# Optimization experiments

Measured on AMD Instinct MI355X. Metric: run time of the kernel, lower is better.

The kernel has to match this reference:

```python
import jax, jax.numpy as jnp
import numpy as np

F_DIM = 256; L = 4; B = 1; H = 160; W = 160; FH = 1024; N = B * H * W

def _ln(x, w, b):
    mu = jnp.mean(x, -1, keepdims=True)
    var = jnp.mean(jnp.square(x - mu), -1, keepdims=True)
    return (x - mu) * jax.lax.rsqrt(var + 1e-5) * w + b

def _conv(x, w, b, groups=1, pad=0):
    y = jax.lax.conv_general_dilated(x, w, (1, 1), [(pad, pad), (pad, pad)],
                                     dimension_numbers=('NCHW', 'OIHW', 'NCHW'),
                                     feature_group_count=groups)
    return y + b[None, :, None, None]

def _wsilu(x):
    return jax.nn.sigmoid(4.0 * x) * x

def setup_inputs() -> dict:
    key = jax.random.key(0)
    ks = iter(jax.random.split(key, 40))
    nk = lambda: next(ks)
    s = 1.0 / np.sqrt(F_DIM).astype(np.float32)
    inp = {}
    inp['x'] = jax.random.normal(nk(), (B, 1, H, W), jnp.float32)
    inp['cin_w1'] = jax.random.normal(nk(), (F_DIM, 1, 1, 1), jnp.float32)
    inp['cin_b1'] = jnp.zeros((F_DIM,), jnp.float32)
    inp['cin_w2'] = jax.random.normal(nk(), (F_DIM, 1, 7, 7), jnp.float32) * 0.15
    inp['cin_b2'] = jnp.zeros((F_DIM,), jnp.float32)
    inp['ln0_w'] = jnp.ones((F_DIM,), jnp.float32); inp['ln0_b'] = jnp.zeros((F_DIM,), jnp.float32)
    inp['ln1_w'] = jnp.ones((L, F_DIM), jnp.float32); inp['ln1_b'] = jnp.zeros((L, F_DIM), jnp.float32)
    inp['ln2_w'] = jnp.ones((L, F_DIM), jnp.float32); inp['ln2_b'] = jnp.zeros((L, F_DIM), jnp.float32)
    for n in ['att_tmk', 'att_tmv', 'att_tmr', 'ffn_tmk', 'ffn_tmr']:
        inp[n] = jax.random.uniform(nk(), (L, F_DIM), jnp.float32)
    inp['att_tf'] = jax.random.normal(nk(), (L, F_DIM), jnp.float32) * 0.5
    # time_decay is stored as -exp(raw) by the module's loader
    inp['att_td'] = -jnp.exp(jax.random.normal(nk(), (L, F_DIM), jnp.float32) * 0.5)
    for n in ['att_kw', 'att_vw', 'att_rw', 'att_ow', 'ffn_rw']:
        inp[n] = jax.random.normal(nk(), (L, F_DIM, F_DIM), jnp.float32) * s
    inp['ffn_kw'] = jax.random.normal(nk(), (L, FH, F_DIM), jnp.float32) * s
    inp['ffn_vw'] = jax.random.normal(nk(), (L, F_DIM, FH), jnp.float32) * (1.0 / np.sqrt(FH).astype(np.float32))
    inp['spa_dw_w'] = jax.random.normal(nk(), (L, F_DIM, 1, 7, 7), jnp.float32) * 0.15
    inp['spa_dw_b'] = jnp.zeros((L, F_DIM), jnp.float32)
    inp['spa_pw_w'] = jax.random.normal(nk(), (L, F_DIM, F_DIM, 1, 1), jnp.float32) * s
    inp['spa_pw_b'] = jnp.zeros((L, F_DIM), jnp.float32)
    st = jnp.zeros((5 * L, N, F_DIM), jnp.float32)
    st = st.at[4::5].add(-1e30)  # pp slots start at -1e30 as in torch init
    inp['state0'] = st
    return inp

def reference(x, cin_w1, cin_b1, cin_w2, cin_b2, ln0_w, ln0_b, ln1_w, ln1_b,
              ln2_w, ln2_b, att_tmk, att_tmv, att_tmr, att_tf, att_td,
              att_kw, att_vw, att_rw, att_ow, ffn_tmk, ffn_tmr, ffn_kw,
              ffn_vw, ffn_rw, spa_dw_w, spa_dw_b, spa_pw_w, spa_pw_b, state0):
    # conv stem: 1x1 -> depthwise 7x7 -> WSiLU
    d = _conv(x, cin_w1, cin_b1)
    d = _wsilu(_conv(d, cin_w2, cin_b2, groups=F_DIM, pad=3))
    d = d.transpose(0, 2, 3, 1).reshape(N, F_DIM)  # 'b f h w -> (b h w) f'
    for i in range(L):
        if i == 0:
            d = _ln(d, ln0_w, ln0_b)
        # --- SA: single-step RWKV WKV ---
        xs = _ln(d, ln1_w[i], ln1_b[i])
        sp = state0[5 * i + 1]
        aa = state0[5 * i + 2]; bb = state0[5 * i + 3]; pp = state0[5 * i + 4]
        xk = xs * att_tmk[i] + sp * (1 - att_tmk[i])
        xv = xs * att_tmv[i] + sp * (1 - att_tmv[i])
        xr = xs * att_tmr[i] + sp * (1 - att_tmr[i])
        r = jax.nn.sigmoid(xr @ att_rw[i].T)
        k = xk @ att_kw[i].T
        v = xv @ att_vw[i].T
        ww = att_tf[i] + k
        p = jnp.maximum(pp, ww)
        e1 = jnp.exp(pp - p); e2 = jnp.exp(ww - p)
        wkv = (e1 * aa + e2 * v) / (e1 * bb + e2)
        d = d + (r * wkv) @ att_ow[i].T
        # --- FF: squared-relu channel mix ---
        xs = _ln(d, ln2_w[i], ln2_b[i])
        sp = state0[5 * i + 0]
        xk = xs * ffn_tmk[i] + sp * (1 - ffn_tmk[i])
        xr = xs * ffn_tmr[i] + sp * (1 - ffn_tmr[i])
        rr = jax.nn.sigmoid(xr @ ffn_rw[i].T)
        kk = jnp.square(jax.nn.relu(xk @ ffn_kw[i].T))
        d = d + rr * (kk @ ffn_vw[i].T)
        # --- spatial residual block ---
        img = d.reshape(B, H, W, F_DIM).transpose(0, 3, 1, 2)
        img = img + _conv(_conv(img, spa_dw_w[i], spa_dw_b[i], groups=F_DIM, pad=3),
                          spa_pw_w[i], spa_pw_b[i])
        d = img.transpose(0, 2, 3, 1).reshape(N, F_DIM)
    return d.reshape(B, H, W, F_DIM).transpose(0, 3, 1, 2)
```

## Files before the change

### kernel.cpp

```cpp
#include <hip/hip_runtime.h>
#include <hip/hip_bf16.h>
#include <cstdint>
#include <cstddef>

#define F_DIMC 256
#define FHC    1024
#define IMGH   160
#define IMGW   160
#define NTOK   25600
#define NLAY   4

using bf16 = __hip_bfloat16;
using f16  = _Float16;
typedef __attribute__((ext_vector_type(8))) short bf16x8;
typedef __attribute__((ext_vector_type(4))) float f32x4;

#define MFMA16(a, b, c) __builtin_amdgcn_mfma_f32_16x16x32_bf16((a), (b), (c), 0, 0, 0)

union H4 { f16 h[4]; uint2 u; };
union Pack4 { bf16 h[4]; uint2 u; };

__global__ void cvt_sp_k(const float* __restrict__ state0, bf16* __restrict__ spb)
{
    const size_t NF = (size_t)NTOK * F_DIMC;
    int y = blockIdx.y;
    int slot = (y < 4) ? 5 * y + 1 : 5 * (y - 4);
    size_t e = ((size_t)blockIdx.x * 256 + threadIdx.x) * 4;
    f32x4 v = *(const f32x4*)(state0 + (size_t)slot * NF + e);
    Pack4 p;
    #pragma unroll
    for (int j = 0; j < 4; ++j) p.h[j] = __float2bfloat16(v[j]);
    *(uint2*)(spb + (size_t)y * NF + e) = p.u;
}

__global__ void prep_mix_k(const float* __restrict__ kw, const float* __restrict__ vw,
                           const float* __restrict__ rw, const float* __restrict__ tmk,
                           const float* __restrict__ tmv, const float* __restrict__ tmr,
                           const float* __restrict__ fkw, const float* __restrict__ ftmk,
                           const float* __restrict__ frw, const float* __restrict__ ftmr,
                           bf16* __restrict__ Wcat, bf16* __restrict__ fkw2,
                           bf16* __restrict__ frw2)
{
    int l = blockIdx.y;
    int idx = blockIdx.x * 256 + threadIdx.x;
    int c = idx & 511, cc = c & 255;
    bool hi2 = c >= 256;
    int r = idx >> 9;
    if (r < 768) {
        const float* W; const float* T; int rr = r;
        if (r < 256)      { W = kw; T = tmk; }
        else if (r < 512) { W = vw; T = tmv; rr = r - 256; }
        else              { W = rw; T = tmr; rr = r - 512; }
        float w = W[(size_t)l * 65536 + rr * 256 + cc];
        float t = T[l * 256 + cc];
        Wcat[(size_t)l * 768 * 512 + (size_t)r * 512 + c] = __float2bfloat16(w * (hi2 ? 1.f - t : t));
    } else if (r < 1792) {
        int rr = r - 768;
        float w = fkw[(size_t)l * 1024 * 256 + rr * 256 + cc];
        float t = ftmk[l * 256 + cc];
        fkw2[(size_t)l * 1024 * 512 + (size_t)rr * 512 + c] = __float2bfloat16(w * (hi2 ? 1.f - t : t));
    } else {
        int rr = r - 1792;
        float w = frw[(size_t)l * 65536 + rr * 256 + cc];
        float t = ftmr[l * 256 + cc];
        frw2[(size_t)l * 256 * 512 + (size_t)rr * 512 + c] = __float2bfloat16(w * (hi2 ? 1.f - t : t));
    }
}

__global__ void cvt3_k(const float* __restrict__ ow, const float* __restrict__ pw,
                       const float* __restrict__ fvw, const float* __restrict__ dww,
                       bf16* __restrict__ owb, bf16* __restrict__ pwb,
                       bf16* __restrict__ fvwb, float* __restrict__ dwT)
{
    int z = blockIdx.y;
    int i = blockIdx.x * 256 + threadIdx.x;
    if (z == 0)      { if (i < 262144)  owb[i]  = __float2bfloat16(ow[i]); }
    else if (z == 1) { if (i < 262144)  pwb[i]  = __float2bfloat16(pw[i]); }
    else if (z == 2) { if (i < 1048576) fvwb[i] = __float2bfloat16(fvw[i]); }
    else {
        if (i < 50176) {
            int f = i & 255; int lt = i >> 8; int t = lt % 49; int l = lt / 49;
            dwT[i] = dww[((size_t)l * F_DIMC + f) * 49 + t];
        }
    }
}

__global__ __launch_bounds__(256)
void stem2_k(const float* __restrict__ x, const float* __restrict__ w1,
             const float* __restrict__ b1, const float* __restrict__ w2,
             const float* __restrict__ b2, f16* __restrict__ d)
{
    __shared__ float wts[49][64];
    __shared__ float w1s[64], b1s[64], b2s[64];
    __shared__ float2 xp[7][22];
    const int tid = threadIdx.x;
    const int f0 = blockIdx.y * 64;
    const int y = blockIdx.x / 10;
    const int x0 = (blockIdx.x % 10) * 16;

    for (int idx = tid; idx < 49 * 64; idx += 256) {
        int t = idx >> 6, fl = idx & 63;
        wts[t][fl] = w2[(f0 + fl) * 49 + t];
    }
    if (tid < 64) {
        w1s[tid] = w1[f0 + tid];
        b1s[tid] = b1[f0 + tid];
        b2s[tid] = b2[f0 + tid];
    }
    for (int p = tid; p < 7 * 22; p += 256) {
        int py = p / 22, px = p % 22;
        int gy = y + py - 3, gx = x0 + px - 3;
        bool ok = (unsigned)gy < IMGH && (unsigned)gx < IMGW;
        xp[py][px] = ok ? make_float2(x[gy * IMGW + gx], 1.f) : make_float2(0.f, 0.f);
    }
    __syncthreads();

    const int fl = tid & 63;
    const int xbase = (tid >> 6) * 4;
    float acc[4] = {0.f, 0.f, 0.f, 0.f}, accw[4] = {0.f, 0.f, 0.f, 0.f};
    #pragma unroll
    for (int ky = 0; ky < 7; ++ky) {
        float2 row[10];
        #pragma unroll
        for (int q = 0; q < 10; ++q) row[q] = xp[ky][xbase + q];
        #pragma unroll
        for (int kx = 0; kx < 7; ++kx) {
            float w = wts[ky * 7 + kx][fl];
            #pragma unroll
            for (int j = 0; j < 4; ++j) {
                acc[j]  = fmaf(row[j + kx].x, w, acc[j]);
                accw[j] = fmaf(row[j + kx].y, w, accw[j]);
            }
        }
    }
    const float w1f = w1s[fl], b1f = b1s[fl], b2f = b2s[fl];
    #pragma unroll
    for (int j = 0; j < 4; ++j) {
        float u = fmaf(w1f, acc[j], fmaf(b1f, accw[j], b2f));
        int pix = y * IMGW + x0 + xbase + j;
        d[(size_t)pix * F_DIMC + f0 + fl] = (f16)(u / (1.f + __expf(-4.f * u)));
    }
}

__device__ __forceinline__ void wave_ln(float* x, const float* __restrict__ w,
                                        const float* __restrict__ b, int lane)
{
    float s = x[0] + x[1] + x[2] + x[3];
    #pragma unroll
    for (int m = 1; m < 64; m <<= 1) s += __shfl_xor(s, m, 64);
    float mu = s * 0.00390625f;
    float t0 = x[0] - mu, t1 = x[1] - mu, t2 = x[2] - mu, t3 = x[3] - mu;
    float v = t0 * t0 + t1 * t1 + t2 * t2 + t3 * t3;
    #pragma unroll
    for (int m = 1; m < 64; m <<= 1) v += __shfl_xor(v, m, 64);
    float inv = rsqrtf(v * 0.00390625f + 1e-5f);
    f32x4 wv = *(const f32x4*)(w + lane * 4);
    f32x4 bv = *(const f32x4*)(b + lane * 4);
    x[0] = t0 * inv * wv[0] + bv[0];
    x[1] = t1 * inv * wv[1] + bv[1];
    x[2] = t2 * inv * wv[2] + bv[2];
    x[3] = t3 * inv * wv[3] + bv[3];
}

__global__ __launch_bounds__(256)
void ln_first_k(f16* __restrict__ d, const float* __restrict__ ln0w,
                const float* __restrict__ ln0b, const float* __restrict__ l1w,
                const float* __restrict__ l1b, bf16* __restrict__ xs)
{
    const int lane = threadIdx.x & 63;
    const int n = blockIdx.x * 4 + (threadIdx.x >> 6);
    const int base = n * F_DIMC + lane * 4;
    H4 hv; hv.u = *(const uint2*)(d + base);
    float xo[4] = {(float)hv.h[0], (float)hv.h[1], (float)hv.h[2], (float)hv.h[3]};
    wave_ln(xo, ln0w, ln0b, lane);
    H4 o;
    #pragma unroll
    for (int j = 0; j < 4; ++j) o.h[j] = (f16)xo[j];
    *(uint2*)(d + base) = o.u;
    wave_ln(xo, l1w, l1b, lane);
    Pack4 p;
    #pragma unroll
    for (int j = 0; j < 4; ++j) p.h[j] = __float2bfloat16(xo[j]);
    *(uint2*)(xs + base) = p.u;
}

__global__ __launch_bounds__(256)
void wkv_k(const f16* __restrict__ G, const float* __restrict__ aa,
           const float* __restrict__ bb, const float* __restrict__ pp,
           const float* __restrict__ tf, bf16* __restrict__ ab)
{
    size_t i = (size_t)blockIdx.x * 256 + threadIdx.x;
    size_t e = i * 4;
    int row = (int)(e >> 8), c = (int)(e & 255);
    const f16* g = G + (size_t)row * 768 + c;
    H4 k4; k4.u = *(const uint2*)(g);
    H4 v4; v4.u = *(const uint2*)(g + 256);
    H4 r4; r4.u = *(const uint2*)(g + 512);
    f32x4 a4 = *(const f32x4*)(aa + e);
    f32x4 b4 = *(const f32x4*)(bb + e);
    f32x4 p4 = *(const f32x4*)(pp + e);
    f32x4 t4 = *(const f32x4*)(tf + c);
    Pack4 po;
    #pragma unroll
    for (int j = 0; j < 4; ++j) {
        float ww = t4[j] + (float)k4.h[j];
        float p = fmaxf(p4[j], ww);
        float e1 = __expf(p4[j] - p);
        float e2 = __expf(ww - p);
        float wkv = (e1 * a4[j] + e2 * (float)v4.h[j]) / (e1 * b4[j] + e2);
        float rs = 1.f / (1.f + __expf(-(float)r4.h[j]));
        po.h[j] = __float2bfloat16(rs * wkv);
    }
    *(uint2*)(ab + e) = po.u;
}

__device__ __forceinline__ void stage_swz16(const bf16* __restrict__ g, int lda,
                                            bf16* lds, int tid)
{
    #pragma unroll
    for (int s = 0; s < 8; ++s) {
        int chunk = s * 256 + tid;
        int row = chunk >> 4, c16 = chunk & 15;
        int gc = c16 ^ (row & 15);
        __builtin_amdgcn_global_load_lds(
            (const __attribute__((address_space(1))) void*)(g + (size_t)row * lda + gc * 8),
            (__attribute__((address_space(3))) void*)(lds + chunk * 8), 16, 0, 0);
    }
}
__device__ __forceinline__ void stage_swz8(const bf16* __restrict__ g, int lda,
                                           bf16* lds, int tid, int nloads)
{
    #pragma unroll
    for (int s = 0; s < 8; ++s) {
        if (s >= nloads) break;
        int chunk = s * 256 + tid;
        int row = chunk >> 3, c = chunk & 7;
        int gc = c ^ (row & 7);
        __builtin_amdgcn_global_load_lds(
            (const __attribute__((address_space(1))) void*)(g + (size_t)row * lda + gc * 8),
            (__attribute__((address_space(3))) void*)(lds + chunk * 8), 16, 0, 0);
    }
}

template<int RB>
__device__ __forceinline__ bf16x8 frag_ld(const bf16* lds, int row, int cb)
{
    constexpr int M = (RB >= 256) ? 15 : (RB / 16 - 1);
    return *(const bf16x8*)((const char*)lds + row * RB + (cb ^ ((row & M) << 4)));
}

template<int EPI, int K, bool SPLITA>
__global__ __launch_bounds__(256, 2)
void gemm128_k(const bf16* __restrict__ A1, const bf16* __restrict__ A2,
               const bf16* __restrict__ Bw, int ldb, int Nout,
               f16* __restrict__ Cf, bf16* __restrict__ Cb)
{
    __shared__ __align__(16) bf16 As[128 * 128];
    __shared__ __align__(16) bf16 Bs[128 * 128];
    const int tid = threadIdx.x, lane = tid & 63, wave = tid >> 6;
    const int wr = wave >> 1, wc = wave & 1;
    const int lr = lane & 15, hi = lane >> 4;
    const int m0 = blockIdx.x * 128, n0 = blockIdx.y * 128;

    f32x4 acc[4][4];
    #pragma unroll
    for (int m = 0; m < 4; ++m)
        #pragma unroll
        for (int n = 0; n < 4; ++n) acc[m][n] = (f32x4){0.f, 0.f, 0.f, 0.f};

    #pragma unroll
    for (int kt = 0; kt < K; kt += 128) {
        const bf16* Ap;
        if constexpr (SPLITA)
            Ap = (kt < 256) ? (A1 + (size_t)m0 * 256 + kt) : (A2 + (size_t)m0 * 256 + (kt - 256));
        else
            Ap = A1 + (size_t)m0 * K + kt;
        stage_swz16(Ap, SPLITA ? 256 : K, As, tid);
        stage_swz16(Bw + (size_t)n0 * ldb + kt, ldb, Bs, tid);
        __syncthreads();
        #pragma unroll
        for (int ks = 0; ks < 4; ++ks) {
            int cb = ks * 64 + hi * 16;
            bf16x8 a[4], b[4];
            #pragma unroll
            for (int mf = 0; mf < 4; ++mf) a[mf] = frag_ld<256>(As, wr * 64 + mf * 16 + lr, cb);
            #pragma unroll
            for (int nf = 0; nf < 4; ++nf) b[nf] = frag_ld<256>(Bs, wc * 64 + nf * 16 + lr, cb);
            #pragma unroll
            for (int mf = 0; mf < 4; ++mf)
                #pragma unroll
                for (int nf = 0; nf < 4; ++nf)
                    acc[mf][nf] = MFMA16(a[mf], b[nf], acc[mf][nf]);
        }
        __syncthreads();
    }

    const int lr0 = hi * 4;
    #pragma unroll
    for (int mf = 0; mf < 4; ++mf)
        #pragma unroll
        for (int nf = 0; nf < 4; ++nf) {
            int col = n0 + wc * 64 + nf * 16 + lr;
            #pragma unroll
            for (int j = 0; j < 4; ++j) {
                int row = m0 + wr * 64 + mf * 16 + lr0 + j;
                size_t cidx = (size_t)row * Nout + col;
                float v = acc[mf][nf][j];
                if constexpr (EPI == 0) Cf[cidx] = (f16)v;
                else if constexpr (EPI == 2) { float t = fmaxf(v, 0.f); Cb[cidx] = __float2bfloat16(t * t); }
            }
        }
}

template<bool BIAS, bool DOLN>
__global__ __launch_bounds__(256, 2)
void gemmln_k(const bf16* __restrict__ A, const bf16* __restrict__ W,
              f16* __restrict__ d, bf16* __restrict__ xs,
              const float* __restrict__ lnw, const float* __restrict__ lnb,
              const float* __restrict__ bias)
{
    __shared__ __align__(16) bf16 As[64 * 64];
    __shared__ __align__(16) bf16 Bs[256 * 64];
    __shared__ float2 lnp[64][4];
    const int tid = threadIdx.x, lane = tid & 63, wave = tid >> 6;
    const int lr = lane & 15, hi = lane >> 4;
    const int m0 = blockIdx.x * 64;

    f32x4 acc[4][4];
    #pragma unroll
    for (int m = 0; m < 4; ++m)
        #pragma unroll
        for (int n = 0; n < 4; ++n) acc[m][n] = (f32x4){0.f, 0.f, 0.f, 0.f};

    #pragma unroll
    for (int kt = 0; kt < 256; kt += 64) {
        stage_swz8(A + (size_t)m0 * 256 + kt, 256, As, tid, 2);
        stage_swz8(W + kt, 256, Bs, tid, 8);
        __syncthreads();
        #pragma unroll
        for (int ks = 0; ks < 2; ++ks) {
            int cb = ks * 64 + hi * 16;
            bf16x8 a[4], b[4];
            #pragma unroll
            for (int mf = 0; mf < 4; ++mf) a[mf] = frag_ld<128>(As, mf * 16 + lr, cb);
            #pragma unroll
            for (int nf = 0; nf < 4; ++nf) b[nf] = frag_ld<128>(Bs, wave * 64 + nf * 16 + lr, cb);
            #pragma unroll
            for (int mf = 0; mf < 4; ++mf)
                #pragma unroll
                for (int nf = 0; nf < 4; ++nf)
                    acc[mf][nf] = MFMA16(a[mf], b[nf], acc[mf][nf]);
        }
        __syncthreads();
    }

    const int lr0 = hi * 4;
    #pragma unroll
    for (int mf = 0; mf < 4; ++mf) {
        #pragma unroll
        for (int j = 0; j < 4; ++j) {
            int row = m0 + mf * 16 + lr0 + j;
            float s = 0.f, q = 0.f;
            #pragma unroll
            for (int nf = 0; nf < 4; ++nf) {
                int col = wave * 64 + nf * 16 + lr;
                size_t ci = (size_t)row * F_DIMC + col;
                float v = acc[mf][nf][j] + (float)d[ci];
                if constexpr (BIAS) v += bias[col];
                acc[mf][nf][j] = v;
                d[ci] = (f16)v;
                s += v; q += v * v;
            }
            if constexpr (DOLN) {
                #pragma unroll
                for (int m = 1; m < 16; m <<= 1) {
                    s += __shfl_xor(s, m, 64);
                    q += __shfl_xor(q, m, 64);
                }
                if (lr == 0) lnp[mf * 16 + lr0 + j][wave] = make_float2(s, q);
            }
        }
    }
    if constexpr (DOLN) {
        __syncthreads();
        #pragma unroll
        for (int mf = 0; mf < 4; ++mf) {
            #pragma unroll
            for (int j = 0; j < 4; ++j) {
                int ri = mf * 16 + lr0 + j;
                float S = 0.f, Q = 0.f;
                #pragma unroll
                for (int w2 = 0; w2 < 4; ++w2) {
                    float2 p = lnp[ri][w2];
                    S += p.x; Q += p.y;
                }
                float mu = S * 0.00390625f;
                float var = Q * 0.00390625f - mu * mu;
                float inv = rsqrtf(var + 1e-5f);
                int row = m0 + ri;
                #pragma unroll
                for (int nf = 0; nf < 4; ++nf) {
                    int col = wave * 64 + nf * 16 + lr;
                    float v = (acc[mf][nf][j] - mu) * inv * lnw[col] + lnb[col];
                    xs[(size_t)row * F_DIMC + col] = __float2bfloat16(v);
                }
            }
        }
    }
}

__global__ __launch_bounds__(256, 2)
void fvwrr_k(const bf16* __restrict__ kkb, const bf16* __restrict__ fvw,
             const bf16* __restrict__ xs, const bf16* __restrict__ sp,
             const bf16* __restrict__ frw2, f16* __restrict__ d)
{
    __shared__ __align__(16) bf16 As[128 * 128];
    __shared__ __align__(16) bf16 Bs[128 * 128];
    const int tid = threadIdx.x, lane = tid & 63, wave = tid >> 6;
    const int wr = wave >> 1, wc = wave & 1;
    const int lr = lane & 15, hi = lane >> 4;
    const int m0 = blockIdx.x * 128, n0 = blockIdx.y * 128;

    f32x4 arr[4][4], am[4][4];
    #pragma unroll
    for (int m = 0; m < 4; ++m)
        #pragma unroll
        for (int n = 0; n < 4; ++n) {
            arr[m][n] = (f32x4){0.f, 0.f, 0.f, 0.f};
            am[m][n]  = (f32x4){0.f, 0.f, 0.f, 0.f};
        }

    #pragma unroll
    for (int kt = 0; kt < 512; kt += 128) {
        const bf16* Ap = (kt < 256) ? (xs + (size_t)m0 * 256 + kt) : (sp + (size_t)m0 * 256 + (kt - 256));
        stage_swz16(Ap, 256, As, tid);
        stage_swz16(frw2 + (size_t)n0 * 512 + kt, 512, Bs, tid);
        __syncthreads();
        #pragma unroll
        for (int ks = 0; ks < 4; ++ks) {
            int cb = ks * 64 + hi * 16;
            bf16x8 a[4], b[4];
            #pragma unroll
            for (int mf = 0; mf < 4; ++mf) a[mf] = frag_ld<256>(As, wr * 64 + mf * 16 + lr, cb);
            #pragma unroll
            for (int nf = 0; nf < 4; ++nf) b[nf] = frag_ld<256>(Bs, wc * 64 + nf * 16 + lr, cb);
            #pragma unroll
            for (int mf = 0; mf < 4; ++mf)
                #pragma unroll
                for (int nf = 0; nf < 4; ++nf)
                    arr[mf][nf] = MFMA16(a[mf], b[nf], arr[mf][nf]);
        }
        __syncthreads();
    }
    #pragma unroll
    for (int kt = 0; kt < 1024; kt += 128) {
        stage_swz16(kkb + (size_t)m0 * 1024 + kt, 1024, As, tid);
        stage_swz16(fvw + (size_t)n0 * 1024 + kt, 1024, Bs, tid);
        __syncthreads();
        #pragma unroll
        for (int ks = 0; ks < 4; ++ks) {
            int cb = ks * 64 + hi * 16;
            bf16x8 a[4], b[4];
            #pragma unroll
            for (int mf = 0; mf < 4; ++mf) a[mf] = frag_ld<256>(As, wr * 64 + mf * 16 + lr, cb);
            #pragma unroll
            for (int nf = 0; nf < 4; ++nf) b[nf] = frag_ld<256>(Bs, wc * 64 + nf * 16 + lr, cb);
            #pragma unroll
            for (int mf = 0; mf < 4; ++mf)
                #pragma unroll
                for (int nf = 0; nf < 4; ++nf)
                    am[mf][nf] = MFMA16(a[mf], b[nf], am[mf][nf]);
        }
        __syncthreads();
    }

    const int lr0 = hi * 4;
    #pragma unroll
    for (int mf = 0; mf < 4; ++mf)
        #pragma unroll
        for (int nf = 0; nf < 4; ++nf) {
            int col = n0 + wc * 64 + nf * 16 + lr;
            #pragma unroll
            for (int j = 0; j < 4; ++j) {
                int row = m0 + wr * 64 + mf * 16 + lr0 + j;
                size_t cidx = (size_t)row * F_DIMC + col;
                float rr = 1.f / (1.f + __expf(-arr[mf][nf][j]));
                d[cidx] = (f16)((float)d[cidx] + rr * am[mf][nf][j]);
            }
        }
}

__global__ __launch_bounds__(256)
void dwconv2_k(const f16* __restrict__ d, const float* __restrict__ wT,
               const float* __restrict__ bias, bf16* __restrict__ out)
{
    __shared__ float patch[196][64];
    __shared__ float wt[49][64];
    const int lane = threadIdx.x;
    const int ty = threadIdx.y;
    const int f0 = blockIdx.z * 64;
    const int w0 = blockIdx.x * 8, h0 = blockIdx.y * 8;

    for (int t = ty; t < 49; t += 4) wt[t][lane] = wT[t * F_DIMC + f0 + lane];
    for (int p = ty; p < 196; p += 4) {
        int py = p / 14, px = p % 14;
        int gy = h0 + py - 3, gx = w0 + px - 3;
        float v = 0.f;
        if ((unsigned)gy < IMGH && (unsigned)gx < IMGW)
            v = (float)d[(size_t)(gy * IMGW + gx) * F_DIMC + f0 + lane];
        patch[p][lane] = v;
    }
    __syncthreads();

    const float b = bias[f0 + lane];
    #pragma unroll
    for (int rr = 0; rr < 2; ++rr) {
        int ry = ty * 2 + rr;
        float acc8[8];
        #pragma unroll
        for (int px = 0; px < 8; ++px) acc8[px] = b;
        #pragma unroll
        for (int ky = 0; ky < 7; ++ky) {
            float rowv[14];
            #pragma unroll
            for (int c = 0; c < 14; ++c) rowv[c] = patch[(ry + ky) * 14 + c][lane];
            #pragma unroll
            for (int kx = 0; kx < 7; ++kx) {
                float w = wt[ky * 7 + kx][lane];
                #pragma unroll
                for (int px = 0; px < 8; ++px)
                    acc8[px] = fmaf(rowv[px + kx], w, acc8[px]);
            }
        }
        #pragma unroll
        for (int px = 0; px < 8; ++px)
            out[(size_t)((h0 + ry) * IMGW + (w0 + px)) * F_DIMC + f0 + lane] = __float2bfloat16(acc8[px]);
    }
}

__global__ __launch_bounds__(256)
void transpose_out_k(const f16* __restrict__ d, float* __restrict__ out)
{
    __shared__ float tile[32][33];
    const int n0 = blockIdx.x * 32, f0 = blockIdx.y * 32;
    const int tx = threadIdx.x, ty = threadIdx.y;
    for (int r = ty; r < 32; r += 8) tile[r][tx] = (float)d[(size_t)(n0 + r) * F_DIMC + f0 + tx];
    __syncthreads();
    for (int r = ty; r < 32; r += 8) out[(size_t)(f0 + r) * NTOK + n0 + tx] = tile[tx][r];
}

extern "C" void kernel_launch(void* const* d_in, const int* in_sizes, int n_in,
                              void* d_out, int out_size, void* d_ws, size_t ws_size,
                              hipStream_t stream)
{
    if (n_in < 30) return;
    const float* x        = (const float*)d_in[0];
    const float* cin_w1   = (const float*)d_in[1];
    const float* cin_b1   = (const float*)d_in[2];
    const float* cin_w2   = (const float*)d_in[3];
    const float* cin_b2   = (const float*)d_in[4];
    const float* ln0_w    = (const float*)d_in[5];
    const float* ln0_b    = (const float*)d_in[6];
    const float* ln1_w    = (const float*)d_in[7];
    const float* ln1_b    = (const float*)d_in[8];
    const float* ln2_w    = (const float*)d_in[9];
    const float* ln2_b    = (const float*)d_in[10];
    const float* att_tmk  = (const float*)d_in[11];
    const float* att_tmv  = (const float*)d_in[12];
    const float* att_tmr  = (const float*)d_in[13];
    const float* ffn_tmk  = (const float*)d_in[14];
    const float* ffn_tmr  = (const float*)d_in[15];
    const float* att_tf   = (const float*)d_in[16];
    const float* att_kw   = (const float*)d_in[18];
    const float* att_vw   = (const float*)d_in[19];
    const float* att_rw   = (const float*)d_in[20];
    const float* att_ow   = (const float*)d_in[21];
    const float* ffn_rw   = (const float*)d_in[22];
    const float* ffn_kw   = (const float*)d_in[23];
    const float* ffn_vw   = (const float*)d_in[24];
    const float* spa_dw_w = (const float*)d_in[25];
    const float* spa_dw_b = (const float*)d_in[26];
    const float* spa_pw_w = (const float*)d_in[27];
    const float* spa_pw_b = (const float*)d_in[28];
    const float* state0   = (const float*)d_in[29];
    float* out = (float*)d_out;

    const size_t NF = (size_t)NTOK * F_DIMC;
    char* wsp = (char*)d_ws;
    size_t off = 0;
    auto alloc = [&](size_t bytes) -> void* {
        void* p = wsp + off;
        off += (bytes + 255) & ~(size_t)255;
        return p;
    };
    f16*   d_buf = (f16*)alloc(NF * 2);
    bf16*  xs    = (bf16*)alloc(NF * 2);
    f16*   G     = (f16*)alloc((size_t)NTOK * 768 * 2);
    bf16*  ab    = (bf16*)alloc(NF * 2);
    bf16*  kkb   = (bf16*)alloc((size_t)NTOK * FHC * 2);
    bf16*  spb   = (bf16*)alloc(8 * NF * 2);
    bf16*  Wcat  = (bf16*)alloc((size_t)NLAY * 768 * 512 * 2);
    bf16*  fkw2  = (bf16*)alloc((size_t)NLAY * 1024 * 512 * 2);
    bf16*  frw2  = (bf16*)alloc((size_t)NLAY * 256 * 512 * 2);
    bf16*  owb   = (bf16*)alloc((size_t)NLAY * 65536 * 2);
    bf16*  pwb   = (bf16*)alloc((size_t)NLAY * 65536 * 2);
    bf16*  fvwb  = (bf16*)alloc((size_t)NLAY * 262144 * 2);
    float* dwT   = (float*)alloc((size_t)NLAY * 49 * F_DIMC * 4);
    if (off > ws_size) return;

    cvt_sp_k<<<dim3((int)(NF / 1024), 8), dim3(256), 0, stream>>>(state0, spb);
    prep_mix_k<<<dim3(4096, 4), dim3(256), 0, stream>>>(
        att_kw, att_vw, att_rw, att_tmk, att_tmv, att_tmr,
        ffn_kw, ffn_tmk, ffn_rw, ffn_tmr, Wcat, fkw2, frw2);
    cvt3_k<<<dim3(4096, 4), dim3(256), 0, stream>>>(
        att_ow, spa_pw_w, ffn_vw, spa_dw_w, owb, pwb, fvwb, dwT);

    stem2_k<<<dim3(IMGH * 10, 4), dim3(256), 0, stream>>>(x, cin_w1, cin_b1, cin_w2, cin_b2, d_buf);
    ln_first_k<<<dim3(NTOK / 4), dim3(256), 0, stream>>>(d_buf, ln0_w, ln0_b, ln1_w, ln1_b, xs);

    for (int i = 0; i < NLAY; ++i) {
        const float* aa = state0 + (size_t)(5 * i + 2) * NF;
        const float* bb = state0 + (size_t)(5 * i + 3) * NF;
        const float* pp = state0 + (size_t)(5 * i + 4) * NF;
        const float* tf = att_tf + i * F_DIMC;
        const bf16* sp_at = spb + (size_t)i * NF;
        const bf16* sp_ff = spb + (size_t)(4 + i) * NF;
        const bf16* Wcat_i = Wcat + (size_t)i * 768 * 512;
        const bf16* fkw2_i = fkw2 + (size_t)i * 1024 * 512;
        const bf16* frw2_i = frw2 + (size_t)i * 256 * 512;
        const bf16* ow_i   = owb  + (size_t)i * 65536;
        const bf16* pw_i   = pwb  + (size_t)i * 65536;
        const bf16* fvw_i  = fvwb + (size_t)i * 262144;
        const float* dwT_i = dwT + (size_t)i * 49 * F_DIMC;
        const float* dwb_i = spa_dw_b + i * F_DIMC;
        const float* pwbias_i = spa_pw_b + i * F_DIMC;

        gemm128_k<0, 512, true><<<dim3(NTOK / 128, 6), dim3(256), 0, stream>>>(
            xs, sp_at, Wcat_i, 512, 768, G, nullptr);
        wkv_k<<<dim3((int)(NF / 1024)), dim3(256), 0, stream>>>(G, aa, bb, pp, tf, ab);
        gemmln_k<false, true><<<dim3(NTOK / 64), dim3(256), 0, stream>>>(
            ab, ow_i, d_buf, xs, ln2_w + i * F_DIMC, ln2_b + i * F_DIMC, nullptr);
        gemm128_k<2, 512, true><<<dim3(NTOK / 128, 8), dim3(256), 0, stream>>>(
            xs, sp_ff, fkw2_i, 512, 1024, nullptr, kkb);
        fvwrr_k<<<dim3(NTOK / 128, 2), dim3(256), 0, stream>>>(
            kkb, fvw_i, xs, sp_ff, frw2_i, d_buf);
        dwconv2_k<<<dim3(IMGW / 8, IMGH / 8, 4), dim3(64, 4), 0, stream>>>(d_buf, dwT_i, dwb_i, ab);
        if (i < NLAY - 1)
            gemmln_k<true, true><<<dim3(NTOK / 64), dim3(256), 0, stream>>>(
                ab, pw_i, d_buf, xs, ln1_w + (i + 1) * F_DIMC, ln1_b + (i + 1) * F_DIMC, pwbias_i);
        else
            gemmln_k<true, false><<<dim3(NTOK / 64), dim3(256), 0, stream>>>(
                ab, pw_i, d_buf, xs, nullptr, nullptr, pwbias_i);
    }

    transpose_out_k<<<dim3(NTOK / 32, F_DIMC / 32), dim3(32, 8), 0, stream>>>(d_buf, out);
}
```

Measured before the change: 1.999 ms.

## Fuse WKV into output-projection GEMM and read fp32 state directly in GEMMs

The elementwise WKV kernel is folded into the prologue of a new output-projection GEMM, which computes the mixed activations straight into swizzled LDS. This removes the ab round trip and one launch per layer. The separate state-to-bf16 conversion pass and its 8-slice buffer are dropped; the GEMMs now load fp32 state and convert it in registers while staging into LDS. The three prep kernels are merged into one launch. In exchange, the fp32 staging uses plain loads instead of async global-to-LDS copies and reads twice the bytes for the state half of K, which could slow the GEMM mainloops.

```diff
diff --git a/kernel.cpp b/kernel.cpp
--- a/kernel.cpp
+++ b/kernel.cpp
@@ -19,68 +19,56 @@
 
 union H4 { f16 h[4]; uint2 u; };
 union Pack4 { bf16 h[4]; uint2 u; };
-
-__global__ void cvt_sp_k(const float* __restrict__ state0, bf16* __restrict__ spb)
-{
-    const size_t NF = (size_t)NTOK * F_DIMC;
-    int y = blockIdx.y;
-    int slot = (y < 4) ? 5 * y + 1 : 5 * (y - 4);
-    size_t e = ((size_t)blockIdx.x * 256 + threadIdx.x) * 4;
-    f32x4 v = *(const f32x4*)(state0 + (size_t)slot * NF + e);
-    Pack4 p;
-    #pragma unroll
-    for (int j = 0; j < 4; ++j) p.h[j] = __float2bfloat16(v[j]);
-    *(uint2*)(spb + (size_t)y * NF + e) = p.u;
-}
-
-__global__ void prep_mix_k(const float* __restrict__ kw, const float* __restrict__ vw,
-                           const float* __restrict__ rw, const float* __restrict__ tmk,
-                           const float* __restrict__ tmv, const float* __restrict__ tmr,
-                           const float* __restrict__ fkw, const float* __restrict__ ftmk,
-                           const float* __restrict__ frw, const float* __restrict__ ftmr,
-                           bf16* __restrict__ Wcat, bf16* __restrict__ fkw2,
-                           bf16* __restrict__ frw2)
-{
-    int l = blockIdx.y;
+union Pack8 { bf16 h[8]; bf16x8 v; };
+
+__global__ void prep_k(const float* __restrict__ kw, const float* __restrict__ vw,
+                       const float* __restrict__ rw, const float* __restrict__ tmk,
+                       const float* __restrict__ tmv, const float* __restrict__ tmr,
+                       const float* __restrict__ fkw, const float* __restrict__ ftmk,
+                       const float* __restrict__ frw, const float* __restrict__ ftmr,
+                       const float* __restrict__ ow, const float* __restrict__ pw,
+                       const float* __restrict__ fvw, const float* __restrict__ dww,
+                       bf16* __restrict__ Wcat, bf16* __restrict__ fkw2,
+                       bf16* __restrict__ frw2, bf16* __restrict__ owb,
+                       bf16* __restrict__ pwb, bf16* __restrict__ fvwb,
+                       float* __restrict__ dwT)
+{
+    int z = blockIdx.y;
     int idx = blockIdx.x * 256 + threadIdx.x;
-    int c = idx & 511, cc = c & 255;
-    bool hi2 = c >= 256;
-    int r = idx >> 9;
-    if (r < 768) {
-        const float* W; const float* T; int rr = r;
-        if (r < 256)      { W = kw; T = tmk; }
-        else if (r < 512) { W = vw; T = tmv; rr = r - 256; }
-        else              { W = rw; T = tmr; rr = r - 512; }
-        float w = W[(size_t)l * 65536 + rr * 256 + cc];
-        float t = T[l * 256 + cc];
-        Wcat[(size_t)l * 768 * 512 + (size_t)r * 512 + c] = __float2bfloat16(w * (hi2 ? 1.f - t : t));
-    } else if (r < 1792) {
-        int rr = r - 768;
-        float w = fkw[(size_t)l * 1024 * 256 + rr * 256 + cc];
-        float t = ftmk[l * 256 + cc];
-        fkw2[(size_t)l * 1024 * 512 + (size_t)rr * 512 + c] = __float2bfloat16(w * (hi2 ? 1.f - t : t));
+    if (z < 4) {
+        int l = z;
+        int c = idx & 511, cc = c & 255;
+        bool hi2 = c >= 256;
+        int r = idx >> 9;
+        if (r < 768) {
+            const float* W; const float* T; int rr = r;
+            if (r < 256)      { W = kw; T = tmk; }
+            else if (r < 512) { W = vw; T = tmv; rr = r - 256; }
+            else              { W = rw; T = tmr; rr = r - 512; }
+            float w = W[(size_t)l * 65536 + rr * 256 + cc];
+            float t = T[l * 256 + cc];
+            Wcat[(size_t)l * 768 * 512 + (size_t)r * 512 + c] = __float2bfloat16(w * (hi2 ? 1.f - t : t));
+        } else if (r < 1792) {
+            int rr = r - 768;
+            float w = fkw[(size_t)l * 1024 * 256 + rr * 256 + cc];
+            float t = ftmk[l * 256 + cc];
+            fkw2[(size_t)l * 1024 * 512 + (size_t)rr * 512 + c] = __float2bfloat16(w * (hi2 ? 1.f - t : t));
+        } else {
+            int rr = r - 1792;
+            float w = frw[(size_t)l * 65536 + rr * 256 + cc];
+            float t = ftmr[l * 256 + cc];
+            frw2[(size_t)l * 256 * 512 + (size_t)rr * 512 + c] = __float2bfloat16(w * (hi2 ? 1.f - t : t));
+        }
     } else {
-        int rr = r - 1792;
-        float w = frw[(size_t)l * 65536 + rr * 256 + cc];
-        float t = ftmr[l * 256 + cc];
-        frw2[(size_t)l * 256 * 512 + (size_t)rr * 512 + c] = __float2bfloat16(w * (hi2 ? 1.f - t : t));
-    }
-}
-
-__global__ void cvt3_k(const float* __restrict__ ow, const float* __restrict__ pw,
-                       const float* __restrict__ fvw, const float* __restrict__ dww,
-                       bf16* __restrict__ owb, bf16* __restrict__ pwb,
-                       bf16* __restrict__ fvwb, float* __restrict__ dwT)
-{
-    int z = blockIdx.y;
-    int i = blockIdx.x * 256 + threadIdx.x;
-    if (z == 0)      { if (i < 262144)  owb[i]  = __float2bfloat16(ow[i]); }
-    else if (z == 1) { if (i < 262144)  pwb[i]  = __float2bfloat16(pw[i]); }
-    else if (z == 2) { if (i < 1048576) fvwb[i] = __float2bfloat16(fvw[i]); }
-    else {
-        if (i < 50176) {
-            int f = i & 255; int lt = i >> 8; int t = lt % 49; int l = lt / 49;
-            dwT[i] = dww[((size_t)l * F_DIMC + f) * 49 + t];
+        int q = z - 4;
+        if (q == 0)      { if (idx < 262144)  owb[idx]  = __float2bfloat16(ow[idx]); }
+        else if (q == 1) { if (idx < 262144)  pwb[idx]  = __float2bfloat16(pw[idx]); }
+        else if (q == 2) { if (idx < 1048576) fvwb[idx] = __float2bfloat16(fvw[idx]); }
+        else {
+            if (idx < 50176) {
+                int f = idx & 255; int lt = idx >> 8; int t = lt % 49; int l = lt / 49;
+                dwT[idx] = dww[((size_t)l * F_DIMC + f) * 49 + t];
+            }
         }
     }
 }
@@ -184,36 +172,6 @@
     *(uint2*)(xs + base) = p.u;
 }
 
-__global__ __launch_bounds__(256)
-void wkv_k(const f16* __restrict__ G, const float* __restrict__ aa,
-           const float* __restrict__ bb, const float* __restrict__ pp,
-           const float* __restrict__ tf, bf16* __restrict__ ab)
-{
-    size_t i = (size_t)blockIdx.x * 256 + threadIdx.x;
-    size_t e = i * 4;
-    int row = (int)(e >> 8), c = (int)(e & 255);
-    const f16* g = G + (size_t)row * 768 + c;
-    H4 k4; k4.u = *(const uint2*)(g);
-    H4 v4; v4.u = *(const uint2*)(g + 256);
-    H4 r4; r4.u = *(const uint2*)(g + 512);
-    f32x4 a4 = *(const f32x4*)(aa + e);
-    f32x4 b4 = *(const f32x4*)(bb + e);
-    f32x4 p4 = *(const f32x4*)(pp + e);
-    f32x4 t4 = *(const f32x4*)(tf + c);
-    Pack4 po;
-    #pragma unroll
-    for (int j = 0; j < 4; ++j) {
-        float ww = t4[j] + (float)k4.h[j];
-        float p = fmaxf(p4[j], ww);
-        float e1 = __expf(p4[j] - p);
-        float e2 = __expf(ww - p);
-        float wkv = (e1 * a4[j] + e2 * (float)v4.h[j]) / (e1 * b4[j] + e2);
-        float rs = 1.f / (1.f + __expf(-(float)r4.h[j]));
-        po.h[j] = __float2bfloat16(rs * wkv);
-    }
-    *(uint2*)(ab + e) = po.u;
-}
-
 __device__ __forceinline__ void stage_swz16(const bf16* __restrict__ g, int lda,
                                             bf16* lds, int tid)
 {
@@ -225,6 +183,25 @@
         __builtin_amdgcn_global_load_lds(
             (const __attribute__((address_space(1))) void*)(g + (size_t)row * lda + gc * 8),
             (__attribute__((address_space(3))) void*)(lds + chunk * 8), 16, 0, 0);
+    }
+}
+__device__ __forceinline__ void stage_f32_swz16(const float* __restrict__ g, int lda,
+                                                bf16* lds, int tid)
+{
+    #pragma unroll
+    for (int s = 0; s < 8; ++s) {
+        int chunk = s * 256 + tid;
+        int row = chunk >> 4, c16 = chunk & 15;
+        int gc = c16 ^ (row & 15);
+        const float* src = g + (size_t)row * lda + gc * 8;
+        f32x4 a = *(const f32x4*)src;
+        f32x4 b = *(const f32x4*)(src + 4);
+        Pack8 p;
+        #pragma unroll
+        for (int j = 0; j < 4; ++j) p.h[j] = __float2bfloat16(a[j]);
+        #pragma unroll
+        for (int j = 0; j < 4; ++j) p.h[4 + j] = __float2bfloat16(b[j]);
+        *(bf16x8*)(lds + chunk * 8) = p.v;
     }
 }
 __device__ __forceinline__ void stage_swz8(const bf16* __restrict__ g, int lda,
@@ -249,10 +226,10 @@
     return *(const bf16x8*)((const char*)lds + row * RB + (cb ^ ((row & M) << 4)));
 }
 
-template<int EPI, int K, bool SPLITA>
+template<int EPI>
 __global__ __launch_bounds__(256, 2)
-void gemm128_k(const bf16* __restrict__ A1, const bf16* __restrict__ A2,
-               const bf16* __restrict__ Bw, int ldb, int Nout,
+void gemm128_k(const bf16* __restrict__ A1, const float* __restrict__ A2f,
+               const bf16* __restrict__ Bw, int Nout,
                f16* __restrict__ Cf, bf16* __restrict__ Cb)
 {
     __shared__ __align__(16) bf16 As[128 * 128];
@@ -269,14 +246,12 @@
         for (int n = 0; n < 4; ++n) acc[m][n] = (f32x4){0.f, 0.f, 0.f, 0.f};
 
     #pragma unroll
-    for (int kt = 0; kt < K; kt += 128) {
-        const bf16* Ap;
-        if constexpr (SPLITA)
-            Ap = (kt < 256) ? (A1 + (size_t)m0 * 256 + kt) : (A2 + (size_t)m0 * 256 + (kt - 256));
+    for (int kt = 0; kt < 512; kt += 128) {
+        if (kt < 256)
+            stage_swz16(A1 + (size_t)m0 * 256 + kt, 256, As, tid);
         else
-            Ap = A1 + (size_t)m0 * K + kt;
-        stage_swz16(Ap, SPLITA ? 256 : K, As, tid);
-        stage_swz16(Bw + (size_t)n0 * ldb + kt, ldb, Bs, tid);
+            stage_f32_swz16(A2f + (size_t)m0 * 256 + (kt - 256), 256, As, tid);
+        stage_swz16(Bw + (size_t)n0 * 512 + kt, 512, Bs, tid);
         __syncthreads();
         #pragma unroll
         for (int ks = 0; ks < 4; ++ks) {
@@ -307,14 +282,144 @@
                 size_t cidx = (size_t)row * Nout + col;
                 float v = acc[mf][nf][j];
                 if constexpr (EPI == 0) Cf[cidx] = (f16)v;
-                else if constexpr (EPI == 2) { float t = fmaxf(v, 0.f); Cb[cidx] = __float2bfloat16(t * t); }
-            }
-        }
-}
-
-template<bool BIAS, bool DOLN>
+                else { float t = fmaxf(v, 0.f); Cb[cidx] = __float2bfloat16(t * t); }
+            }
+        }
+}
+
 __global__ __launch_bounds__(256, 2)
-void gemmln_k(const bf16* __restrict__ A, const bf16* __restrict__ W,
+void gemmow_k(const f16* __restrict__ G, const float* __restrict__ aa,
+              const float* __restrict__ bb, const float* __restrict__ pp,
+              const float* __restrict__ tf, const bf16* __restrict__ W,
+              f16* __restrict__ d, bf16* __restrict__ xs,
+              const float* __restrict__ lnw, const float* __restrict__ lnb)
+{
+    __shared__ __align__(16) bf16 As[64 * 256];
+    __shared__ __align__(16) bf16 Bs[256 * 64];
+    __shared__ float2 lnp[64][4];
+    const int tid = threadIdx.x, lane = tid & 63, wave = tid >> 6;
+    const int lr = lane & 15, hi = lane >> 4;
+    const int m0 = blockIdx.x * 64;
+
+    stage_swz8(W, 256, Bs, tid, 8);
+
+    #pragma unroll
+    for (int rb = 0; rb < 4; ++rb) {
+        int r = rb * 16 + (tid >> 4);
+        int row = m0 + r;
+        const f16* g = G + (size_t)row * 768;
+        const size_t sb = (size_t)row * F_DIMC;
+        #pragma unroll
+        for (int j = 0; j < 4; ++j) {
+            int c = (tid & 15) * 4 + j * 64;
+            H4 k4; k4.u = *(const uint2*)(g + c);
+            H4 v4; v4.u = *(const uint2*)(g + 256 + c);
+            H4 r4; r4.u = *(const uint2*)(g + 512 + c);
+            f32x4 a4 = *(const f32x4*)(aa + sb + c);
+            f32x4 b4 = *(const f32x4*)(bb + sb + c);
+            f32x4 p4 = *(const f32x4*)(pp + sb + c);
+            f32x4 t4 = *(const f32x4*)(tf + c);
+            Pack4 po;
+            #pragma unroll
+            for (int q = 0; q < 4; ++q) {
+                float ww = t4[q] + (float)k4.h[q];
+                float p = fmaxf(p4[q], ww);
+                float e1 = __expf(p4[q] - p);
+                float e2 = __expf(ww - p);
+                float wkv = (e1 * a4[q] + e2 * (float)v4.h[q]) / (e1 * b4[q] + e2);
+                float rs = 1.f / (1.f + __expf(-(float)r4.h[q]));
+                po.h[q] = __float2bfloat16(rs * wkv);
+            }
+            int chunk = c >> 3;
+            int off = (c & 4) ? 8 : 0;
+            *(uint2*)((char*)As + r * 512 + ((chunk ^ (r & 15)) << 4) + off) = po.u;
+        }
+    }
+    __syncthreads();
+
+    f32x4 acc[4][4];
+    #pragma unroll
+    for (int m = 0; m < 4; ++m)
+        #pragma unroll
+        for (int n = 0; n < 4; ++n) acc[m][n] = (f32x4){0.f, 0.f, 0.f, 0.f};
+
+    #pragma unroll
+    for (int kt = 0; kt < 256; kt += 64) {
+        if (kt > 0) {
+            stage_swz8(W + kt, 256, Bs, tid, 8);
+            __syncthreads();
+        }
+        #pragma unroll
+        for (int ks = 0; ks < 2; ++ks) {
+            int cbA = kt * 2 + ks * 64 + hi * 16;
+            int cbB = ks * 64 + hi * 16;
+            bf16x8 a[4], b[4];
+            #pragma unroll
+            for (int mf = 0; mf < 4; ++mf) a[mf] = frag_ld<512>(As, mf * 16 + lr, cbA);
+            #pragma unroll
+            for (int nf = 0; nf < 4; ++nf) b[nf] = frag_ld<128>(Bs, wave * 64 + nf * 16 + lr, cbB);
+            #pragma unroll
+            for (int mf = 0; mf < 4; ++mf)
+                #pragma unroll
+                for (int nf = 0; nf < 4; ++nf)
+                    acc[mf][nf] = MFMA16(a[mf], b[nf], acc[mf][nf]);
+        }
+        __syncthreads();
+    }
+
+    const int lr0 = hi * 4;
+    #pragma unroll
+    for (int mf = 0; mf < 4; ++mf) {
+        #pragma unroll
+        for (int j = 0; j < 4; ++j) {
+            int row = m0 + mf * 16 + lr0 + j;
+            float s = 0.f, q = 0.f;
+            #pragma unroll
+            for (int nf = 0; nf < 4; ++nf) {
+                int col = wave * 64 + nf * 16 + lr;
+                size_t ci = (size_t)row * F_DIMC + col;
+                float v = acc[mf][nf][j] + (float)d[ci];
+                acc[mf][nf][j] = v;
+                d[ci] = (f16)v;
+                s += v; q += v * v;
+            }
+            #pragma unroll
+            for (int m = 1; m < 16; m <<= 1) {
+                s += __shfl_xor(s, m, 64);
+                q += __shfl_xor(q, m, 64);
+            }
+            if (lr == 0) lnp[mf * 16 + lr0 + j][wave] = make_float2(s, q);
+        }
+    }
+    __syncthreads();
+    #pragma unroll
+    for (int mf = 0; mf < 4; ++mf) {
+        #pragma unroll
+        for (int j = 0; j < 4; ++j) {
+            int ri = mf * 16 + lr0 + j;
+            float S = 0.f, Q = 0.f;
+            #pragma unroll
+            for (int w2 = 0; w2 < 4; ++w2) {
+                float2 p = lnp[ri][w2];
+                S += p.x; Q += p.y;
+            }
+            float mu = S * 0.00390625f;
+            float var = Q * 0.00390625f - mu * mu;
+            float inv = rsqrtf(var + 1e-5f);
+            int row = m0 + ri;
+            #pragma unroll
+            for (int nf = 0; nf < 4; ++nf) {
+                int col = wave * 64 + nf * 16 + lr;
+                float v = (acc[mf][nf][j] - mu) * inv * lnw[col] + lnb[col];
+                xs[(size_t)row * F_DIMC + col] = __float2bfloat16(v);
+            }
+        }
+    }
+}
+
+template<bool DOLN>
+__global__ __launch_bounds__(256, 2)
+void gemmpw_k(const bf16* __restrict__ A, const bf16* __restrict__ W,
               f16* __restrict__ d, bf16* __restrict__ xs,
               const float* __restrict__ lnw, const float* __restrict__ lnb,
               const float* __restrict__ bias)
@@ -365,8 +470,7 @@
             for (int nf = 0; nf < 4; ++nf) {
                 int col = wave * 64 + nf * 16 + lr;
                 size_t ci = (size_t)row * F_DIMC + col;
-                float v = acc[mf][nf][j] + (float)d[ci];
-                if constexpr (BIAS) v += bias[col];
+                float v = acc[mf][nf][j] + (float)d[ci] + bias[col];
                 acc[mf][nf][j] = v;
                 d[ci] = (f16)v;
                 s += v; q += v * v;
@@ -411,7 +515,7 @@
 
 __global__ __launch_bounds__(256, 2)
 void fvwrr_k(const bf16* __restrict__ kkb, const bf16* __restrict__ fvw,
-             const bf16* __restrict__ xs, const bf16* __restrict__ sp,
+             const bf16* __restrict__ xs, const float* __restrict__ spf,
              const bf16* __restrict__ frw2, f16* __restrict__ d)
 {
     __shared__ __align__(16) bf16 As[128 * 128];
@@ -432,8 +536,10 @@
 
     #pragma unroll
     for (int kt = 0; kt < 512; kt += 128) {
-        const bf16* Ap = (kt < 256) ? (xs + (size_t)m0 * 256 + kt) : (sp + (size_t)m0 * 256 + (kt - 256));
-        stage_swz16(Ap, 256, As, tid);
+        if (kt < 256)
+            stage_swz16(xs + (size_t)m0 * 256 + kt, 256, As, tid);
+        else
+            stage_f32_swz16(spf + (size_t)m0 * 256 + (kt - 256), 256, As, tid);
         stage_swz16(frw2 + (size_t)n0 * 512 + kt, 512, Bs, tid);
         __syncthreads();
         #pragma unroll
@@ -598,7 +704,6 @@
     f16*   G     = (f16*)alloc((size_t)NTOK * 768 * 2);
     bf16*  ab    = (bf16*)alloc(NF * 2);
     bf16*  kkb   = (bf16*)alloc((size_t)NTOK * FHC * 2);
-    bf16*  spb   = (bf16*)alloc(8 * NF * 2);
     bf16*  Wcat  = (bf16*)alloc((size_t)NLAY * 768 * 512 * 2);
     bf16*  fkw2  = (bf16*)alloc((size_t)NLAY * 1024 * 512 * 2);
     bf16*  frw2  = (bf16*)alloc((size_t)NLAY * 256 * 512 * 2);
@@ -608,23 +713,22 @@
     float* dwT   = (float*)alloc((size_t)NLAY * 49 * F_DIMC * 4);
     if (off > ws_size) return;
 
-    cvt_sp_k<<<dim3((int)(NF / 1024), 8), dim3(256), 0, stream>>>(state0, spb);
-    prep_mix_k<<<dim3(4096, 4), dim3(256), 0, stream>>>(
+    prep_k<<<dim3(4096, 8), dim3(256), 0, stream>>>(
         att_kw, att_vw, att_rw, att_tmk, att_tmv, att_tmr,
-        ffn_kw, ffn_tmk, ffn_rw, ffn_tmr, Wcat, fkw2, frw2);
-    cvt3_k<<<dim3(4096, 4), dim3(256), 0, stream>>>(
-        att_ow, spa_pw_w, ffn_vw, spa_dw_w, owb, pwb, fvwb, dwT);
+        ffn_kw, ffn_tmk, ffn_rw, ffn_tmr,
+        att_ow, spa_pw_w, ffn_vw, spa_dw_w,
+        Wcat, fkw2, frw2, owb, pwb, fvwb, dwT);
 
     stem2_k<<<dim3(IMGH * 10, 4), dim3(256), 0, stream>>>(x, cin_w1, cin_b1, cin_w2, cin_b2, d_buf);
     ln_first_k<<<dim3(NTOK / 4), dim3(256), 0, stream>>>(d_buf, ln0_w, ln0_b, ln1_w, ln1_b, xs);
 
     for (int i = 0; i < NLAY; ++i) {
-        const float* aa = state0 + (size_t)(5 * i + 2) * NF;
-        const float* bb = state0 + (size_t)(5 * i + 3) * NF;
-        const float* pp = state0 + (size_t)(5 * i + 4) * NF;
-        const float* tf = att_tf + i * F_DIMC;
-        const bf16* sp_at = spb + (size_t)i * NF;
-        const bf16* sp_ff = spb + (size_t)(4 + i) * NF;
+        const float* sp_ff = state0 + (size_t)(5 * i + 0) * NF;
+        const float* sp_at = state0 + (size_t)(5 * i + 1) * NF;
+        const float* aa    = state0 + (size_t)(5 * i + 2) * NF;
+        const float* bb    = state0 + (size_t)(5 * i + 3) * NF;
+        const float* pp    = state0 + (size_t)(5 * i + 4) * NF;
+        const float* tf    = att_tf + i * F_DIMC;
         const bf16* Wcat_i = Wcat + (size_t)i * 768 * 512;
         const bf16* fkw2_i = fkw2 + (size_t)i * 1024 * 512;
         const bf16* frw2_i = frw2 + (size_t)i * 256 * 512;
@@ -635,21 +739,20 @@
         const float* dwb_i = spa_dw_b + i * F_DIMC;
         const float* pwbias_i = spa_pw_b + i * F_DIMC;
 
-        gemm128_k<0, 512, true><<<dim3(NTOK / 128, 6), dim3(256), 0, stream>>>(
-            xs, sp_at, Wcat_i, 512, 768, G, nullptr);
-        wkv_k<<<dim3((int)(NF / 1024)), dim3(256), 0, stream>>>(G, aa, bb, pp, tf, ab);
-        gemmln_k<false, true><<<dim3(NTOK / 64), dim3(256), 0, stream>>>(
-            ab, ow_i, d_buf, xs, ln2_w + i * F_DIMC, ln2_b + i * F_DIMC, nullptr);
-        gemm128_k<2, 512, true><<<dim3(NTOK / 128, 8), dim3(256), 0, stream>>>(
-            xs, sp_ff, fkw2_i, 512, 1024, nullptr, kkb);
+        gemm128_k<0><<<dim3(NTOK / 128, 6), dim3(256), 0, stream>>>(
+            xs, sp_at, Wcat_i, 768, G, nullptr);
+        gemmow_k<<<dim3(NTOK / 64), dim3(256), 0, stream>>>(
+            G, aa, bb, pp, tf, ow_i, d_buf, xs, ln2_w + i * F_DIMC, ln2_b + i * F_DIMC);
+        gemm128_k<2><<<dim3(NTOK / 128, 8), dim3(256), 0, stream>>>(
+            xs, sp_ff, fkw2_i, 1024, nullptr, kkb);
         fvwrr_k<<<dim3(NTOK / 128, 2), dim3(256), 0, stream>>>(
             kkb, fvw_i, xs, sp_ff, frw2_i, d_buf);
         dwconv2_k<<<dim3(IMGW / 8, IMGH / 8, 4), dim3(64, 4), 0, stream>>>(d_buf, dwT_i, dwb_i, ab);
         if (i < NLAY - 1)
-            gemmln_k<true, true><<<dim3(NTOK / 64), dim3(256), 0, stream>>>(
+            gemmpw_k<true><<<dim3(NTOK / 64), dim3(256), 0, stream>>>(
                 ab, pw_i, d_buf, xs, ln1_w + (i + 1) * F_DIMC, ln1_b + (i + 1) * F_DIMC, pwbias_i);
         else
-            gemmln_k<true, false><<<dim3(NTOK / 64), dim3(256), 0, stream>>>(
+            gemmpw_k<false><<<dim3(NTOK / 64), dim3(256), 0, stream>>>(
                 ab, pw_i, d_buf, xs, nullptr, nullptr, pwbias_i);
     }
 
```

Measured after the change: 2.013 ms. Within noise of the previous version (+0.7%).
